# Kernel optimization log

Measured on AMD Instinct MI355X. Metric: run time of the kernel, lower is better.

Reference implementation:

```python
import jax, jax.numpy as jnp
import numpy as np

E, D, A = 1024, 1024, 512

def setup_inputs() -> dict:
    key = jax.random.key(0)
    ks = jax.random.split(key, 8)
    B, S = 32, 2048
    s_e = 1.0 / np.sqrt(E)
    s_d = 1.0 / np.sqrt(D)
    s_a = 1.0 / np.sqrt(A)
    return {
        "encoder_outputs": jax.random.normal(ks[0], (B, S, E), jnp.float32),
        "decoder_hidden": jax.random.normal(ks[1], (B, D), jnp.float32),
        "We": jax.random.uniform(ks[2], (E, A), jnp.float32, -s_e, s_e),
        "be": jax.random.uniform(ks[3], (A,), jnp.float32, -s_e, s_e),
        "Wd": jax.random.uniform(ks[4], (D, A), jnp.float32, -s_d, s_d),
        "bd": jax.random.uniform(ks[5], (A,), jnp.float32, -s_d, s_d),
        "v_w": jax.random.uniform(ks[6], (A,), jnp.float32, -s_a, s_a),
        "v_b": jax.random.uniform(ks[7], (), jnp.float32, -s_a, s_a),
    }

def reference(encoder_outputs, decoder_hidden, We, be, Wd, bd, v_w, v_b):
    # encoder_energy: [B,S,A]; decoder_energy: [B,1,A]
    enc_e = jnp.einsum('bse,ea->bsa', encoder_outputs, We) + be
    dec_e = (decoder_hidden @ Wd + bd)[:, None, :]
    energy = jnp.tanh(enc_e + dec_e)                     # [B,S,A]
    scores = jnp.einsum('bsa,a->bs', energy, v_w) + v_b  # [B,S]
    attn = jax.nn.softmax(scores, axis=1)                # [B,S]
    context = jnp.einsum('bs,bse->be', attn, encoder_outputs)  # [B,E]
    return context, attn
```

## Files before the change

kernel.cpp:

```cpp
#include <hip/hip_runtime.h>
#include <math.h>

#define E_DIM 1024
#define D_DIM 1024
#define A_DIM 512
#define B_NUM 32
#define S_DIM 2048
#define M_DIM (B_NUM * S_DIM)

typedef unsigned short ushort;
typedef short short8 __attribute__((ext_vector_type(8)));
typedef float f32x4 __attribute__((ext_vector_type(4)));
typedef unsigned short ushort4v __attribute__((ext_vector_type(4)));

typedef const void __attribute__((address_space(1))) cglobal_t;
typedef void __attribute__((address_space(3))) lds_t;

__device__ __forceinline__ void gload_lds16(const void* g, void* l) {
    __builtin_amdgcn_global_load_lds((cglobal_t*)g, (lds_t*)l, 16, 0, 0);
}

__device__ __forceinline__ ushort f2bf(float x) {
    unsigned u = __float_as_uint(x);
    u += 0x7FFF + ((u >> 16) & 1);
    return (ushort)(u >> 16);
}

__device__ __forceinline__ unsigned cvt_pk_bf16(float lo, float hi) {
    unsigned r;
    asm("v_cvt_pk_bf16_f32 %0, %1, %2" : "=v"(r) : "v"(lo), "v"(hi));
    return r;
}

__device__ __forceinline__ float fast_tanh(float x) {
    const float e = __expf(2.0f * x);
    return 1.0f - 2.0f * __builtin_amdgcn_rcpf(e + 1.0f);
}

__global__ __launch_bounds__(256) void k0c_cvt_enc(
    const float* __restrict__ enc, ushort* __restrict__ ebf) {
    const size_t stride = (size_t)gridDim.x * 256;
    const size_t n8 = (size_t)M_DIM * E_DIM / 8;
    for (size_t i = (size_t)blockIdx.x * 256 + threadIdx.x; i < n8; i += stride) {
        const float4 a = *reinterpret_cast<const float4*>(enc + i * 8);
        const float4 b = *reinterpret_cast<const float4*>(enc + i * 8 + 4);
        *reinterpret_cast<int4*>(ebf + i * 8) =
            make_int4(cvt_pk_bf16(a.x, a.y), cvt_pk_bf16(a.z, a.w),
                      cvt_pk_bf16(b.x, b.y), cvt_pk_bf16(b.z, b.w));
    }
}

__global__ __launch_bounds__(256) void k0_dec_energy(
    const float* __restrict__ dh, const float* __restrict__ Wd,
    const float* __restrict__ bd, const float* __restrict__ be,
    float* __restrict__ dec2) {
    __shared__ float sdh[D_DIM];
    const int b = blockIdx.y;
    const int t = threadIdx.x;
    for (int i = t; i < D_DIM; i += 256) sdh[i] = dh[b * D_DIM + i];
    __syncthreads();
    const int a = blockIdx.x * 256 + t;
    float acc = bd[a] + be[a];
#pragma unroll 8
    for (int e = 0; e < D_DIM; ++e) acc += sdh[e] * Wd[(size_t)e * A_DIM + a];
    dec2[b * A_DIM + a] = acc;
}

__global__ __launch_bounds__(256) void k0b_cvt_we(
    const float* __restrict__ We, ushort* __restrict__ Wt) {
    const int n = blockIdx.x;
    const int k0 = threadIdx.x * 4;
    ushort4v v;
#pragma unroll
    for (int j = 0; j < 4; ++j) v[j] = f2bf(We[(size_t)(k0 + j) * A_DIM + n]);
    *reinterpret_cast<ushort4v*>(&Wt[(size_t)n * E_DIM + k0]) = v;
}

#define BM2 256
#define BN2 256
#define BK2 32
#define NT2 (E_DIM / BK2)
#define BUFU 16384

__global__ __launch_bounds__(512, 2) void k1_mfma_8w(
    const ushort* __restrict__ ebf, const ushort* __restrict__ Wt,
    const float* __restrict__ dec2, const float* __restrict__ v_w,
    float* __restrict__ pscores) {
    __shared__ ushort L[3 * BUFU];

    const int t = threadIdx.x;
    const int l = t & 63;
    const int w = t >> 6;
    const int wm = w >> 2;
    const int wn = w & 3;
    const int fr = l & 15;
    const int kg = l >> 4;

    const int o = ((blockIdx.x & 7) << 6) | (blockIdx.x >> 3);
    const int x = o >> 1, ny = o & 1;
    const int row0 = x * BM2;
    const int n0 = ny * BN2;
    const int b = row0 >> 11;

    const int sA0 = t, sA1 = 512 + t;
    const int rA0 = sA0 >> 2, rA1 = sA1 >> 2;
    const int cA0 = (sA0 & 3) ^ ((rA0 >> 1) & 3);
    const int cA1 = (sA1 & 3) ^ ((rA1 >> 1) & 3);
    const ushort* srcA0 = ebf + (size_t)(row0 + rA0) * E_DIM + cA0 * 8;
    const ushort* srcA1 = ebf + (size_t)(row0 + rA1) * E_DIM + cA1 * 8;
    const ushort* srcB0 = Wt + (size_t)(n0 + rA0) * E_DIM + cA0 * 8;
    const ushort* srcB1 = Wt + (size_t)(n0 + rA1) * E_DIM + cA1 * 8;
    const int ldsA0 = w * 512;
    const int ldsA1 = 4096 + w * 512;
    const int ldsB0 = 8192 + w * 512;
    const int ldsB1 = 8192 + 4096 + w * 512;

#define STAGE2(cb, kt)                                             \
    {                                                              \
        const int ko = (kt) * BK2;                                 \
        ushort* base = L + (cb) * BUFU;                            \
        gload_lds16(srcA0 + ko, base + ldsA0);                     \
        gload_lds16(srcA1 + ko, base + ldsA1);                     \
        gload_lds16(srcB0 + ko, base + ldsB0);                     \
        gload_lds16(srcB1 + ko, base + ldsB1);                     \
    }

    f32x4 acc[8][4];
#pragma unroll
    for (int i = 0; i < 8; ++i)
#pragma unroll
        for (int j = 0; j < 4; ++j) acc[i][j] = (f32x4){0.f, 0.f, 0.f, 0.f};

    STAGE2(0, 0);
    STAGE2(1, 1);
    asm volatile("s_waitcnt vmcnt(4)" ::: "memory");
    __builtin_amdgcn_s_barrier();

    int cbuf = 0, pbuf = 2;
    for (int kt = 0; kt < NT2; ++kt) {
        if (kt < NT2 - 2) STAGE2(pbuf, kt + 2);

        const ushort* Ab = L + cbuf * BUFU;
        const ushort* Bb = Ab + 8192;
        short8 af[8], bf[4];
#pragma unroll
        for (int i = 0; i < 8; ++i) {
            const int r = wm * 128 + i * 16 + fr;
            af[i] = *reinterpret_cast<const short8*>(
                Ab + r * 32 + ((kg ^ ((r >> 1) & 3)) << 3));
        }
#pragma unroll
        for (int j = 0; j < 4; ++j) {
            const int r = wn * 64 + j * 16 + fr;
            bf[j] = *reinterpret_cast<const short8*>(
                Bb + r * 32 + ((kg ^ ((r >> 1) & 3)) << 3));
        }
        __builtin_amdgcn_s_setprio(1);
#pragma unroll
        for (int i = 0; i < 8; ++i)
#pragma unroll
            for (int j = 0; j < 4; ++j)
                acc[i][j] = __builtin_amdgcn_mfma_f32_16x16x32_bf16(af[i], bf[j], acc[i][j], 0, 0, 0);
        __builtin_amdgcn_s_setprio(0);

        if (kt < NT2 - 2) {
            asm volatile("s_waitcnt vmcnt(4)" ::: "memory");
        } else if (kt == NT2 - 2) {
            asm volatile("s_waitcnt vmcnt(0)" ::: "memory");
        }
        __builtin_amdgcn_s_barrier();

        cbuf = (cbuf == 2) ? 0 : cbuf + 1;
        pbuf = (pbuf == 2) ? 0 : pbuf + 1;
    }

    float rowsum[8][4];
#pragma unroll
    for (int i = 0; i < 8; ++i)
#pragma unroll
        for (int r = 0; r < 4; ++r) rowsum[i][r] = 0.0f;

#pragma unroll
    for (int j = 0; j < 4; ++j) {
        const int ag = n0 + wn * 64 + j * 16 + fr;
        const float bias = dec2[b * A_DIM + ag];
        const float vw = v_w[ag];
#pragma unroll
        for (int i = 0; i < 8; ++i)
#pragma unroll
            for (int r = 0; r < 4; ++r)
                rowsum[i][r] += fast_tanh(acc[i][j][r] + bias) * vw;
    }
#pragma unroll
    for (int m = 1; m < 16; m <<= 1)
#pragma unroll
        for (int i = 0; i < 8; ++i)
#pragma unroll
            for (int r = 0; r < 4; ++r)
                rowsum[i][r] += __shfl_xor(rowsum[i][r], m, 64);

    float* red = reinterpret_cast<float*>(L);
    if (fr == 0) {
#pragma unroll
        for (int i = 0; i < 8; ++i)
#pragma unroll
            for (int r = 0; r < 4; ++r)
                red[(wm * 128 + i * 16 + kg * 4 + r) * 4 + wn] = rowsum[i][r];
    }
    __syncthreads();
    if (t < BM2) {
        const float s = red[t * 4] + red[t * 4 + 1] + red[t * 4 + 2] + red[t * 4 + 3];
        pscores[(size_t)(row0 + t) * 2 + ny] = s;
    }
}

#define BM 128
#define BN 128
#define BK 32
#define PAD 40
__global__ __launch_bounds__(256, 2) void k1_mfma_reg(
    const float* __restrict__ enc, const ushort* __restrict__ Wt,
    const float* __restrict__ dec2, const float* __restrict__ v_w,
    float* __restrict__ pscores) {
    __shared__ ushort As[2][BM][PAD];
    __shared__ ushort Bs[2][BN][PAD];

    const int t = threadIdx.x;
    const int l = t & 63;
    const int w = t >> 6;
    const int wm = w >> 1, wn = w & 1;
    const int fr = l & 15;
    const int kg = l >> 4;

    const int o = ((blockIdx.x & 7) << 8) | (blockIdx.x >> 3);
    const int x = o >> 2, y = o & 3;
    const int row0 = x * BM;
    const int n0 = y * BN;
    const int b = row0 >> 11;

    const int srow = t >> 1;
    const int skh = (t & 1) * 16;

    const float* Ag = enc + (size_t)(row0 + srow) * E_DIM + skh;
    const ushort* Bg = Wt + (size_t)(n0 + srow) * E_DIM + skh;

    f32x4 acc[4][4];
#pragma unroll
    for (int i = 0; i < 4; ++i)
#pragma unroll
        for (int j = 0; j < 4; ++j) acc[i][j] = (f32x4){0.f, 0.f, 0.f, 0.f};

    float4 pa[4];
    int4 pb[2];

#define STAGE_LOAD(k0)                                              \
    {                                                               \
        pa[0] = *reinterpret_cast<const float4*>(Ag + (k0));        \
        pa[1] = *reinterpret_cast<const float4*>(Ag + (k0) + 4);    \
        pa[2] = *reinterpret_cast<const float4*>(Ag + (k0) + 8);    \
        pa[3] = *reinterpret_cast<const float4*>(Ag + (k0) + 12);   \
        pb[0] = *reinterpret_cast<const int4*>(Bg + (k0));          \
        pb[1] = *reinterpret_cast<const int4*>(Bg + (k0) + 8);      \
    }

#define STAGE_WRITE(buf)                                                  \
    {                                                                     \
        unsigned uu[8];                                                   \
        _Pragma("unroll") for (int q = 0; q < 4; ++q) {                   \
            uu[2 * q] = cvt_pk_bf16(pa[q].x, pa[q].y);                    \
            uu[2 * q + 1] = cvt_pk_bf16(pa[q].z, pa[q].w);                \
        }                                                                 \
        *reinterpret_cast<int4*>(&As[buf][srow][skh]) =                   \
            make_int4(uu[0], uu[1], uu[2], uu[3]);                        \
        *reinterpret_cast<int4*>(&As[buf][srow][skh + 8]) =               \
            make_int4(uu[4], uu[5], uu[6], uu[7]);                        \
        *reinterpret_cast<int4*>(&Bs[buf][srow][skh]) = pb[0];            \
        *reinterpret_cast<int4*>(&Bs[buf][srow][skh + 8]) = pb[1];        \
    }

    STAGE_LOAD(0);
    STAGE_WRITE(0);
    __syncthreads();

    for (int kt = 0; kt < E_DIM / BK; ++kt) {
        const int cur = kt & 1;
        if (kt < E_DIM / BK - 1) STAGE_LOAD((kt + 1) * BK);

        short8 af[4], bf[4];
#pragma unroll
        for (int i = 0; i < 4; ++i)
            af[i] = *reinterpret_cast<const short8*>(&As[cur][wm * 64 + i * 16 + fr][kg * 8]);
#pragma unroll
        for (int j = 0; j < 4; ++j)
            bf[j] = *reinterpret_cast<const short8*>(&Bs[cur][wn * 64 + j * 16 + fr][kg * 8]);
#pragma unroll
        for (int i = 0; i < 4; ++i)
#pragma unroll
            for (int j = 0; j < 4; ++j)
                acc[i][j] = __builtin_amdgcn_mfma_f32_16x16x32_bf16(af[i], bf[j], acc[i][j], 0, 0, 0);

        if (kt < E_DIM / BK - 1) STAGE_WRITE(cur ^ 1);
        __syncthreads();
    }

    float rowsum[4][4];
#pragma unroll
    for (int i = 0; i < 4; ++i)
#pragma unroll
        for (int r = 0; r < 4; ++r) rowsum[i][r] = 0.0f;
#pragma unroll
    for (int j = 0; j < 4; ++j) {
        const int ag = n0 + wn * 64 + j * 16 + fr;
        const float bias = dec2[b * A_DIM + ag];
        const float vw = v_w[ag];
#pragma unroll
        for (int i = 0; i < 4; ++i)
#pragma unroll
            for (int r = 0; r < 4; ++r)
                rowsum[i][r] += fast_tanh(acc[i][j][r] + bias) * vw;
    }
#pragma unroll
    for (int m = 1; m < 16; m <<= 1)
#pragma unroll
        for (int i = 0; i < 4; ++i)
#pragma unroll
            for (int r = 0; r < 4; ++r)
                rowsum[i][r] += __shfl_xor(rowsum[i][r], m, 64);

    __syncthreads();
    float* red = reinterpret_cast<float*>(&As[0][0][0]);
    if (fr == 0) {
#pragma unroll
        for (int i = 0; i < 4; ++i)
#pragma unroll
            for (int r = 0; r < 4; ++r)
                red[(wm * 64 + i * 16 + kg * 4 + r) * 2 + wn] = rowsum[i][r];
    }
    __syncthreads();
    if (t < BM)
        pscores[(size_t)(row0 + t) * 4 + y] = red[t * 2] + red[t * 2 + 1];
}

__global__ __launch_bounds__(256) void k2_softmax(
    const float* __restrict__ pscores, const float* __restrict__ v_b,
    float* __restrict__ attn_out, int W) {
    __shared__ float sc[S_DIM];
    __shared__ float red[8];
    const int b = blockIdx.x;
    const int t = threadIdx.x;
    const int wave = t >> 6, lane = t & 63;
    const float vb = v_b[0];

    float lmax = -1e30f;
    for (int s = t; s < S_DIM; s += 256) {
        float v = vb;
        for (int c = 0; c < W; ++c) v += pscores[(size_t)(b * S_DIM + s) * W + c];
        sc[s] = v;
        lmax = fmaxf(lmax, v);
    }
#pragma unroll
    for (int off = 32; off > 0; off >>= 1) lmax = fmaxf(lmax, __shfl_down(lmax, off, 64));
    if (lane == 0) red[wave] = lmax;
    __syncthreads();
    const float bmax = fmaxf(fmaxf(red[0], red[1]), fmaxf(red[2], red[3]));

    float lsum = 0.0f;
    for (int s = t; s < S_DIM; s += 256) {
        const float e = expf(sc[s] - bmax);
        sc[s] = e;
        lsum += e;
    }
#pragma unroll
    for (int off = 32; off > 0; off >>= 1) lsum += __shfl_down(lsum, off, 64);
    if (lane == 0) red[4 + wave] = lsum;
    __syncthreads();
    const float inv = 1.0f / (red[4] + red[5] + red[6] + red[7]);
    for (int s = t; s < S_DIM; s += 256) attn_out[b * S_DIM + s] = sc[s] * inv;
}

#define SC_CHUNK 128
#define N_SC (S_DIM / SC_CHUNK)
__global__ __launch_bounds__(128) void k3_ctx_bf16(
    const ushort* __restrict__ ebf, const float* __restrict__ attn,
    float* __restrict__ pctx) {
    const int b = blockIdx.y;
    const int scb = blockIdx.x;
    const int t = threadIdx.x;
    const int s0 = scb * SC_CHUNK;
    float acc[8];
#pragma unroll
    for (int j = 0; j < 8; ++j) acc[j] = 0.0f;
    const ushort* base = ebf + (size_t)(b * S_DIM + s0) * E_DIM + t * 8;
#pragma unroll 4
    for (int s = 0; s < SC_CHUNK; ++s) {
        const float wgt = attn[b * S_DIM + s0 + s];
        const int4 v = *reinterpret_cast<const int4*>(base + (size_t)s * E_DIM);
        const unsigned* u = reinterpret_cast<const unsigned*>(&v);
#pragma unroll
        for (int j = 0; j < 4; ++j) {
            acc[2 * j] += wgt * __uint_as_float(u[j] << 16);
            acc[2 * j + 1] += wgt * __uint_as_float(u[j] & 0xffff0000u);
        }
    }
    float* dst = &pctx[(size_t)(b * N_SC + scb) * E_DIM + t * 8];
    *reinterpret_cast<float4*>(dst) = make_float4(acc[0], acc[1], acc[2], acc[3]);
    *reinterpret_cast<float4*>(dst + 4) = make_float4(acc[4], acc[5], acc[6], acc[7]);
}

__global__ __launch_bounds__(256) void k3_ctx_partial(
    const float* __restrict__ enc, const float* __restrict__ attn,
    float* __restrict__ pctx) {
    const int b = blockIdx.y;
    const int scb = blockIdx.x;
    const int t = threadIdx.x;
    const int s0 = scb * SC_CHUNK;
    float4 acc = {0.0f, 0.0f, 0.0f, 0.0f};
    const float4* encv =
        reinterpret_cast<const float4*>(enc + (size_t)(b * S_DIM + s0) * E_DIM);
#pragma unroll 4
    for (int s = 0; s < SC_CHUNK; ++s) {
        const float w = attn[b * S_DIM + s0 + s];
        const float4 v = encv[(size_t)s * (E_DIM / 4) + t];
        acc.x += w * v.x;
        acc.y += w * v.y;
        acc.z += w * v.z;
        acc.w += w * v.w;
    }
    *reinterpret_cast<float4*>(&pctx[(size_t)(b * N_SC + scb) * E_DIM + t * 4]) = acc;
}

__global__ __launch_bounds__(256) void k4_ctx_reduce(
    const float* __restrict__ pctx, float* __restrict__ ctx) {
    const int b = blockIdx.x;
    const int t = threadIdx.x;
    float4 acc = {0.0f, 0.0f, 0.0f, 0.0f};
#pragma unroll
    for (int s = 0; s < N_SC; ++s) {
        const float4 v = *reinterpret_cast<const float4*>(
            &pctx[(size_t)(b * N_SC + s) * E_DIM + t * 4]);
        acc.x += v.x;
        acc.y += v.y;
        acc.z += v.z;
        acc.w += v.w;
    }
    *reinterpret_cast<float4*>(&ctx[(size_t)b * E_DIM + t * 4]) = acc;
}

extern "C" void kernel_launch(void* const* d_in, const int* in_sizes, int n_in,
                              void* d_out, int out_size, void* d_ws, size_t ws_size,
                              hipStream_t stream) {
    (void)in_sizes; (void)n_in; (void)out_size;
    const float* enc = (const float*)d_in[0];
    const float* dh  = (const float*)d_in[1];
    const float* We  = (const float*)d_in[2];
    const float* be  = (const float*)d_in[3];
    const float* Wd  = (const float*)d_in[4];
    const float* bd  = (const float*)d_in[5];
    const float* vw  = (const float*)d_in[6];
    const float* vb  = (const float*)d_in[7];

    float* out = (float*)d_out;
    float* ctx_out = out;
    float* attn_out = out + B_NUM * E_DIM;

    const size_t NEED = 138477568ULL;

    if (ws_size >= NEED) {
        char* W = (char*)d_ws;
        ushort* ebf    = (ushort*)W;
        ushort* Wt     = (ushort*)(W + 134217728);
        float* dec2    = (float*)(W + 135266304);
        float* pscores = (float*)(W + 135331840);
        float* pctx    = (float*)(W + 136380416);

        k0c_cvt_enc<<<dim3(2048), 256, 0, stream>>>(enc, ebf);
        k0_dec_energy<<<dim3(2, 32), 256, 0, stream>>>(dh, Wd, bd, be, dec2);
        k0b_cvt_we<<<dim3(A_DIM), 256, 0, stream>>>(We, Wt);
        k1_mfma_8w<<<dim3((M_DIM / BM2) * (A_DIM / BN2)), 512, 0, stream>>>(
            ebf, Wt, dec2, vw, pscores);
        k2_softmax<<<dim3(B_NUM), 256, 0, stream>>>(pscores, vb, attn_out, 2);
        k3_ctx_bf16<<<dim3(N_SC, B_NUM), 128, 0, stream>>>(ebf, attn_out, pctx);
        k4_ctx_reduce<<<dim3(B_NUM), 256, 0, stream>>>(pctx, ctx_out);
    } else {
        float* ws = (float*)d_ws;
        float* dec2    = ws;
        float* pscores = ws + 16384;
        float* pctx    = ws + 16384 + 262144;
        ushort* Wt     = (ushort*)(ws + 16384 + 262144 + 524288);

        k0_dec_energy<<<dim3(2, 32), 256, 0, stream>>>(dh, Wd, bd, be, dec2);
        k0b_cvt_we<<<dim3(A_DIM), 256, 0, stream>>>(We, Wt);
        k1_mfma_reg<<<dim3((M_DIM / BM) * (A_DIM / BN)), 256, 0, stream>>>(
            enc, Wt, dec2, vw, pscores);
        k2_softmax<<<dim3(B_NUM), 256, 0, stream>>>(pscores, vb, attn_out, 4);
        k3_ctx_partial<<<dim3(N_SC, B_NUM), 256, 0, stream>>>(enc, attn_out, pctx);
        k4_ctx_reduce<<<dim3(B_NUM), 256, 0, stream>>>(pctx, ctx_out);
    }
}
```

Measured before the change: 244.9 us.

## Load A fragments directly into registers, stage only B through LDS

Replaces the 8-wave 256x256 GEMM kernel with a 4-wave 128x256 kernel. Each wave now loads its A (encoder bf16) fragments straight from global memory into registers, double-buffered across k steps, and only B (weights) goes through double-buffered LDS. This is meant to cut LDS traffic and LDS footprint and raise occupancy. The cost is that A is no longer shared through LDS: every wave reads the full 128-row A tile from global/L2, and the global loads are 16-byte strided rows that may be less coalesced.

```diff
diff --git a/kernel.cpp b/kernel.cpp
--- a/kernel.cpp
+++ b/kernel.cpp
@@ -76,54 +76,54 @@
     *reinterpret_cast<ushort4v*>(&Wt[(size_t)n * E_DIM + k0]) = v;
 }
 
-#define BM2 256
-#define BN2 256
-#define BK2 32
-#define NT2 (E_DIM / BK2)
-#define BUFU 16384
-
-__global__ __launch_bounds__(512, 2) void k1_mfma_8w(
+#define BM3 128
+#define BN3 256
+#define NT3 32
+
+__global__ __launch_bounds__(256, 2) void k1_mfma_areg(
     const ushort* __restrict__ ebf, const ushort* __restrict__ Wt,
     const float* __restrict__ dec2, const float* __restrict__ v_w,
     float* __restrict__ pscores) {
-    __shared__ ushort L[3 * BUFU];
+    __shared__ ushort Bsu[2 * 8192];
 
     const int t = threadIdx.x;
     const int l = t & 63;
     const int w = t >> 6;
-    const int wm = w >> 2;
-    const int wn = w & 3;
     const int fr = l & 15;
     const int kg = l >> 4;
 
-    const int o = ((blockIdx.x & 7) << 6) | (blockIdx.x >> 3);
+    const int o = ((blockIdx.x & 7) << 7) | (blockIdx.x >> 3);
     const int x = o >> 1, ny = o & 1;
-    const int row0 = x * BM2;
-    const int n0 = ny * BN2;
+    const int row0 = x * BM3;
+    const int n0 = ny * BN3;
     const int b = row0 >> 11;
 
-    const int sA0 = t, sA1 = 512 + t;
-    const int rA0 = sA0 >> 2, rA1 = sA1 >> 2;
-    const int cA0 = (sA0 & 3) ^ ((rA0 >> 1) & 3);
-    const int cA1 = (sA1 & 3) ^ ((rA1 >> 1) & 3);
-    const ushort* srcA0 = ebf + (size_t)(row0 + rA0) * E_DIM + cA0 * 8;
-    const ushort* srcA1 = ebf + (size_t)(row0 + rA1) * E_DIM + cA1 * 8;
-    const ushort* srcB0 = Wt + (size_t)(n0 + rA0) * E_DIM + cA0 * 8;
-    const ushort* srcB1 = Wt + (size_t)(n0 + rA1) * E_DIM + cA1 * 8;
-    const int ldsA0 = w * 512;
-    const int ldsA1 = 4096 + w * 512;
-    const int ldsB0 = 8192 + w * 512;
-    const int ldsB1 = 8192 + 4096 + w * 512;
-
-#define STAGE2(cb, kt)                                             \
-    {                                                              \
-        const int ko = (kt) * BK2;                                 \
-        ushort* base = L + (cb) * BUFU;                            \
-        gload_lds16(srcA0 + ko, base + ldsA0);                     \
-        gload_lds16(srcA1 + ko, base + ldsA1);                     \
-        gload_lds16(srcB0 + ko, base + ldsB0);                     \
-        gload_lds16(srcB1 + ko, base + ldsB1);                     \
-    }
+    const ushort* Abase = ebf + (size_t)(row0 + fr) * E_DIM + kg * 8;
+
+#define LOAD_A(dst, ktv)                                                       \
+    {                                                                          \
+        _Pragma("unroll") for (int i = 0; i < 8; ++i)                          \
+            dst[i] = *reinterpret_cast<const short8*>(                         \
+                Abase + (size_t)i * 16 * E_DIM + (ktv) * 32);                  \
+    }
+
+    const ushort* BsrcQ[4];
+#pragma unroll
+    for (int q = 0; q < 4; ++q) {
+        const int row = (w * 4 + q) * 16 + (l >> 2);
+        const int c = (l & 3) ^ ((row >> 1) & 3);
+        BsrcQ[q] = Wt + (size_t)(n0 + row) * E_DIM + c * 8;
+    }
+
+#define STAGE_B(cb, ktv)                                                       \
+    {                                                                          \
+        _Pragma("unroll") for (int q = 0; q < 4; ++q)                          \
+            gload_lds16(BsrcQ[q] + (ktv) * 32,                                 \
+                        Bsu + (cb) * 8192 + (w * 4 + q) * 512);                \
+    }
+
+    const int rB = w * 64 + fr;
+    const int bbyte = rB * 64 + ((kg ^ ((rB >> 1) & 3)) * 16);
 
     f32x4 acc[8][4];
 #pragma unroll
@@ -131,48 +131,42 @@
 #pragma unroll
         for (int j = 0; j < 4; ++j) acc[i][j] = (f32x4){0.f, 0.f, 0.f, 0.f};
 
-    STAGE2(0, 0);
-    STAGE2(1, 1);
-    asm volatile("s_waitcnt vmcnt(4)" ::: "memory");
+    short8 aP[8], aN[8];
+
+#define ITER(acur, anext, cb, ktv, PF)                                         \
+    {                                                                          \
+        if (PF) {                                                              \
+            STAGE_B((cb) ^ 1, (ktv) + 1);                                      \
+            LOAD_A(anext, (ktv) + 1);                                          \
+        }                                                                      \
+        short8 bf[4];                                                          \
+        _Pragma("unroll") for (int j = 0; j < 4; ++j)                          \
+            bf[j] = *reinterpret_cast<const short8*>(                          \
+                (const char*)Bsu + (cb) * 16384 + bbyte + j * 1024);           \
+        __builtin_amdgcn_s_setprio(1);                                         \
+        _Pragma("unroll") for (int i = 0; i < 8; ++i)                          \
+            _Pragma("unroll") for (int j = 0; j < 4; ++j)                      \
+                acc[i][j] = __builtin_amdgcn_mfma_f32_16x16x32_bf16(           \
+                    acur[i], bf[j], acc[i][j], 0, 0, 0);                       \
+        __builtin_amdgcn_s_setprio(0);                                         \
+        if (PF) {                                                              \
+            asm volatile("s_waitcnt vmcnt(8)" ::: "memory");                   \
+            __builtin_amdgcn_s_barrier();                                      \
+        }                                                                      \
+    }
+
+    STAGE_B(0, 0);
+    LOAD_A(aP, 0);
+    asm volatile("s_waitcnt vmcnt(8)" ::: "memory");
     __builtin_amdgcn_s_barrier();
 
-    int cbuf = 0, pbuf = 2;
-    for (int kt = 0; kt < NT2; ++kt) {
-        if (kt < NT2 - 2) STAGE2(pbuf, kt + 2);
-
-        const ushort* Ab = L + cbuf * BUFU;
-        const ushort* Bb = Ab + 8192;
-        short8 af[8], bf[4];
-#pragma unroll
-        for (int i = 0; i < 8; ++i) {
-            const int r = wm * 128 + i * 16 + fr;
-            af[i] = *reinterpret_cast<const short8*>(
-                Ab + r * 32 + ((kg ^ ((r >> 1) & 3)) << 3));
-        }
-#pragma unroll
-        for (int j = 0; j < 4; ++j) {
-            const int r = wn * 64 + j * 16 + fr;
-            bf[j] = *reinterpret_cast<const short8*>(
-                Bb + r * 32 + ((kg ^ ((r >> 1) & 3)) << 3));
-        }
-        __builtin_amdgcn_s_setprio(1);
-#pragma unroll
-        for (int i = 0; i < 8; ++i)
-#pragma unroll
-            for (int j = 0; j < 4; ++j)
-                acc[i][j] = __builtin_amdgcn_mfma_f32_16x16x32_bf16(af[i], bf[j], acc[i][j], 0, 0, 0);
-        __builtin_amdgcn_s_setprio(0);
-
-        if (kt < NT2 - 2) {
-            asm volatile("s_waitcnt vmcnt(4)" ::: "memory");
-        } else if (kt == NT2 - 2) {
-            asm volatile("s_waitcnt vmcnt(0)" ::: "memory");
-        }
-        __builtin_amdgcn_s_barrier();
-
-        cbuf = (cbuf == 2) ? 0 : cbuf + 1;
-        pbuf = (pbuf == 2) ? 0 : pbuf + 1;
-    }
+#pragma unroll
+    for (int kt = 0; kt < NT3 - 2; kt += 2) {
+        ITER(aP, aN, 0, kt, true);
+        ITER(aN, aP, 1, kt + 1, true);
+    }
+    ITER(aP, aN, 0, NT3 - 2, true);
+    ITER(aN, aP, 1, NT3 - 1, false);
 
     float rowsum[8][4];
 #pragma unroll
@@ -182,7 +176,7 @@
 
 #pragma unroll
     for (int j = 0; j < 4; ++j) {
-        const int ag = n0 + wn * 64 + j * 16 + fr;
+        const int ag = n0 + w * 64 + j * 16 + fr;
         const float bias = dec2[b * A_DIM + ag];
         const float vw = v_w[ag];
 #pragma unroll
@@ -199,16 +193,17 @@
             for (int r = 0; r < 4; ++r)
                 rowsum[i][r] += __shfl_xor(rowsum[i][r], m, 64);
 
-    float* red = reinterpret_cast<float*>(L);
+    __syncthreads();
+    float* red = reinterpret_cast<float*>(Bsu);
     if (fr == 0) {
 #pragma unroll
         for (int i = 0; i < 8; ++i)
 #pragma unroll
             for (int r = 0; r < 4; ++r)
-                red[(wm * 128 + i * 16 + kg * 4 + r) * 4 + wn] = rowsum[i][r];
-    }
-    __syncthreads();
-    if (t < BM2) {
+                red[(i * 16 + kg * 4 + r) * 4 + w] = rowsum[i][r];
+    }
+    __syncthreads();
+    if (t < BM3) {
         const float s = red[t * 4] + red[t * 4 + 1] + red[t * 4 + 2] + red[t * 4 + 3];
         pscores[(size_t)(row0 + t) * 2 + ny] = s;
     }
@@ -476,7 +471,7 @@
         k0c_cvt_enc<<<dim3(2048), 256, 0, stream>>>(enc, ebf);
         k0_dec_energy<<<dim3(2, 32), 256, 0, stream>>>(dh, Wd, bd, be, dec2);
         k0b_cvt_we<<<dim3(A_DIM), 256, 0, stream>>>(We, Wt);
-        k1_mfma_8w<<<dim3((M_DIM / BM2) * (A_DIM / BN2)), 512, 0, stream>>>(
+        k1_mfma_areg<<<dim3((M_DIM / BM3) * (A_DIM / BN3)), 256, 0, stream>>>(
             ebf, Wt, dec2, vw, pscores);
         k2_softmax<<<dim3(B_NUM), 256, 0, stream>>>(pscores, vb, attn_out, 2);
         k3_ctx_bf16<<<dim3(N_SC, B_NUM), 128, 0, stream>>>(ebf, attn_out, pctx);
```

After: 324.6 us. 32.6% more time.
